# Optimization experiments

Hardware: AMD Instinct MI355X
Metric: run time of the kernel (lower is better)

The kernel has to match this reference:

```python
import jax, jax.numpy as jnp
from jax import lax
import numpy as np

DN = ('NCHW', 'OIHW', 'NCHW')

def conv(x, w, b, stride, pad):
    y = lax.conv_general_dilated(x, w, (stride, stride), [(pad, pad), (pad, pad)], dimension_numbers=DN)
    return y + b[None, :, None, None]

def conv_t(x, w, b):
    # torch ConvTranspose2d(k=4, s=2, p=1); w is torch layout [Cin, Cout, 4, 4]
    wf = jnp.flip(w, (2, 3)).transpose(1, 0, 2, 3)  # -> OIHW
    y = lax.conv_general_dilated(x, wf, (1, 1), [(2, 2), (2, 2)], lhs_dilation=(2, 2), dimension_numbers=DN)
    return y + b[None, :, None, None]

def setup_inputs() -> dict:
    key = jax.random.key(0)
    ks = jax.random.split(key, 20)
    B, C_in, H, W = 8, 1, 512, 512
    hid, zc, K = 64, 64, 512
    s = 0.05
    inp = {
        'x': jax.random.uniform(ks[0], (B, C_in, H, W), jnp.float32),
        # encoder: three 4x4 s2 convs + one 3x3 s1 conv
        'enc_w1': jax.random.normal(ks[1], (hid, C_in, 4, 4), jnp.float32) * s,
        'enc_b1': jnp.zeros((hid,), jnp.float32),
        'enc_w2': jax.random.normal(ks[2], (hid, hid, 4, 4), jnp.float32) * s,
        'enc_b2': jnp.zeros((hid,), jnp.float32),
        'enc_w3': jax.random.normal(ks[3], (hid, hid, 4, 4), jnp.float32) * s,
        'enc_b3': jnp.zeros((hid,), jnp.float32),
        'enc_w4': jax.random.normal(ks[4], (zc, hid, 3, 3), jnp.float32) * s,
        'enc_b4': jnp.zeros((zc,), jnp.float32),
        # codebook, uniform(-1/K, 1/K) as in torch init
        'codebook': jax.random.uniform(ks[5], (K, zc), jnp.float32, -1.0 / K, 1.0 / K),
        # decoder: 3x3 s1 conv + three 4x4 s2 conv-transposes (torch [Cin,Cout,kH,kW] layout)
        'dec_w1': jax.random.normal(ks[6], (hid, zc, 3, 3), jnp.float32) * s,
        'dec_b1': jnp.zeros((hid,), jnp.float32),
        'dec_tw1': jax.random.normal(ks[7], (hid, hid, 4, 4), jnp.float32) * s,
        'dec_tb1': jnp.zeros((hid,), jnp.float32),
        'dec_tw2': jax.random.normal(ks[8], (hid, hid, 4, 4), jnp.float32) * s,
        'dec_tb2': jnp.zeros((hid,), jnp.float32),
        'dec_tw3': jax.random.normal(ks[9], (hid, C_in, 4, 4), jnp.float32) * s,
        'dec_tb3': jnp.zeros((C_in,), jnp.float32),
    }
    return inp

def _forward(x, enc_w1, enc_b1, enc_w2, enc_b2, enc_w3, enc_b3, enc_w4, enc_b4,
             codebook, dec_w1, dec_b1, dec_tw1, dec_tb1, dec_tw2, dec_tb2, dec_tw3, dec_tb3):
    # ---- encoder ----
    h = jax.nn.relu(conv(x, enc_w1, enc_b1, 2, 1))
    h = jax.nn.relu(conv(h, enc_w2, enc_b2, 2, 1))
    h = jax.nn.relu(conv(h, enc_w3, enc_b3, 2, 1))
    z = conv(h, enc_w4, enc_b4, 1, 1)  # [B, zc, H/8, W/8]
    # ---- vector quantizer ----
    B, C, Hh, Ww = z.shape
    z_flat = z.transpose(0, 2, 3, 1).reshape(-1, C)  # [N, C]
    dist = (jnp.sum(z_flat ** 2, axis=1, keepdims=True)
            + jnp.sum(codebook ** 2, axis=1)
            - 2.0 * z_flat @ codebook.T)  # [N, K]
    idx = jnp.argmin(dist, axis=1)
    z_q = codebook[idx].reshape(B, Hh, Ww, C).transpose(0, 3, 1, 2)
    sg = lax.stop_gradient
    vq_loss = jnp.mean((sg(z_q) - z) ** 2) + 0.25 * jnp.mean((z_q - sg(z)) ** 2)
    z_q = z + sg(z_q - z)  # straight-through
    # ---- decoder ----
    d = jax.nn.relu(conv(z_q, dec_w1, dec_b1, 1, 1))
    d = jax.nn.relu(conv_t(d, dec_tw1, dec_tb1))
    d = jax.nn.relu(conv_t(d, dec_tw2, dec_tb2))
    x_hat = jax.nn.sigmoid(conv_t(d, dec_tw3, dec_tb3))
    return x_hat, vq_loss

def reference(x, enc_w1, enc_b1, enc_w2, enc_b2, enc_w3, enc_b3, enc_w4, enc_b4,
              codebook, dec_w1, dec_b1, dec_tw1, dec_tb1, dec_tw2, dec_tb2, dec_tw3, dec_tb3):
    return _forward(x, enc_w1, enc_b1, enc_w2, enc_b2, enc_w3, enc_b3, enc_w4, enc_b4,
                    codebook, dec_w1, dec_b1, dec_tw1, dec_tb1, dec_tw2, dec_tb2, dec_tw3, dec_tb3)
```

## Files before the change

kernel.cpp:

```cpp
#include <hip/hip_runtime.h>
#include <math.h>


typedef __bf16 bf16x8_t __attribute__((ext_vector_type(8)));
typedef _Float16 f16x8_t __attribute__((ext_vector_type(8)));
typedef float f32x4_t __attribute__((ext_vector_type(4)));
typedef _Float16 h2_t __attribute__((ext_vector_type(2)));

union FragU { uint4 u; bf16x8_t b; };
union Frag16 { uint4 u; f16x8_t h; };

__device__ inline f32x4_t mfma16(bf16x8_t a, bf16x8_t b, f32x4_t c) {
    return __builtin_amdgcn_mfma_f32_16x16x32_bf16(a, b, c, 0, 0, 0);
}
__device__ inline f32x4_t mfma16h(f16x8_t a, f16x8_t b, f32x4_t c) {
    return __builtin_amdgcn_mfma_f32_16x16x32_f16(a, b, c, 0, 0, 0);
}

__device__ inline void gl_lds16(const void* g, void* l) {
    __builtin_amdgcn_global_load_lds((const __attribute__((address_space(1))) void*)g,
                                     (__attribute__((address_space(3))) void*)l, 16, 0, 0);
}

__device__ inline unsigned bf16rne(float f) {
    unsigned u = __float_as_uint(f);
    u += 0x7FFFu + ((u >> 16) & 1u);
    return u >> 16;
}
__device__ inline unsigned pack2(float lo, float hi) {
    return bf16rne(lo) | (bf16rne(hi) << 16);
}
__device__ inline unsigned pack2h(float lo, float hi) {
    union { h2_t h; unsigned u; } r;
    r.h[0] = (_Float16)lo; r.h[1] = (_Float16)hi;
    return r.u;
}
__device__ inline unsigned short f16bits(float v) {
    union { _Float16 h; unsigned short s; } x; x.h = (_Float16)v; return x.s;
}
__device__ inline float f16lo(unsigned u) {
    union { unsigned u; h2_t h; } x; x.u = u; return (float)x.h[0];
}
__device__ inline float f16hi(unsigned u) {
    union { unsigned u; h2_t h; } x; x.u = u; return (float)x.h[1];
}
__device__ inline float bl(unsigned u) { return __uint_as_float(u << 16); }
__device__ inline float bh(unsigned u) { return __uint_as_float(u & 0xffff0000u); }

#if defined(__has_builtin)
#if __has_builtin(__builtin_amdgcn_fdot2)
#define HAS_FDOT2 1
#endif
#endif

__device__ inline float dot2h(unsigned x, unsigned w, float a) {
#ifdef HAS_FDOT2
    union { unsigned u; h2_t h; } ax, bw;
    ax.u = x; bw.u = w;
    return __builtin_amdgcn_fdot2(ax.h, bw.h, a, false);
#else
    union { unsigned u; _Float16 h[2]; } ax, bw;
    ax.u = x; bw.u = w;
    a = fmaf((float)ax.h[0], (float)bw.h[0], a);
    return fmaf((float)ax.h[1], (float)bw.h[1], a);
#endif
}
__device__ inline float dot8(uint4 x, uint4 w, float a) {
    a = dot2h(x.x, w.x, a); a = dot2h(x.y, w.y, a);
    a = dot2h(x.z, w.z, a); a = dot2h(x.w, w.w, a);
    return a;
}

template<int NR, int KW_, int SW, int CIC, int SPT, int NT, int OUTM>
__global__ __launch_bounds__(256) void conv_mfma(
    const unsigned short* __restrict__ in, const unsigned short* __restrict__ wp,
    const float* __restrict__ bias, void* __restrict__ outp,
    int Hp, int Wp, int PS, int nchunks, int Cout, int ncog,
    int Hpo, int Wpo, int relu)
{
    constexpr int W_ST = SW * (SPT - 1) + KW_;
    constexpr int SLOTS_PP = CIC / 8;
    constexpr int ROW_SLOTS = W_ST * SLOTS_PP;
    constexpr int SEGS = (ROW_SLOTS + 63) / 64;
    constexpr int KT = NR * KW_;
    constexpr int CSTEPS = CIC / 32;
    __shared__ __align__(16) unsigned short sh[NR * W_ST * CIC];

    int t = threadIdx.x, lane = t & 63, wv = t >> 6;
    int bx = blockIdx.x;
    int owt = bx;
    int ohg = blockIdx.y;
    int bz = blockIdx.z; int nb = bz / ncog; int cog = bz % ncog;
    int ow0 = owt * SPT;
    int row0 = SW * ohg;
    int col0 = SW * ow0;
    int coh = wv & 1;
    int sph = wv >> 1;
    int m = lane & 15, g = lane >> 4;

    f32x4_t acc[2][NT];
#pragma unroll
    for (int a = 0; a < 2; ++a)
#pragma unroll
        for (int u2 = 0; u2 < NT; ++u2) acc[a][u2] = (f32x4_t){0.f, 0.f, 0.f, 0.f};

    for (int ch = 0; ch < nchunks; ++ch) {
        if (ch) __syncthreads();
        for (int u_ = wv; u_ < NR * SEGS; u_ += 4) {
            int r = u_ / SEGS, seg = u_ - r * SEGS;
            int slot = seg * 64 + lane;
            int p = slot / SLOTS_PP;
            int uu = slot & (SLOTS_PP - 1);
            if (p < W_ST) {
                int su = (uu - (p & 7)) & (SLOTS_PP - 1);
                const unsigned short* gsrc = in +
                    (((size_t)nb * Hp + (row0 + r)) * Wp + (col0 + p)) * PS + ch * CIC + su * 8;
                unsigned short* ldst = sh + ((size_t)(r * ROW_SLOTS + seg * 64 + lane)) * 8;
                gl_lds16(gsrc, ldst);
            }
        }
        __syncthreads();
        int sbase = ch * (KT * CSTEPS);
#pragma unroll
        for (int tap = 0; tap < KT; ++tap) {
            const int r_l = tap / KW_, kwp = tap % KW_;
#pragma unroll
            for (int cs = 0; cs < CSTEPS; ++cs) {
                int s = sbase + tap * CSTEPS + cs;
                const uint4* wr = (const uint4*)wp + (size_t)(s * 4 + g) * Cout + cog * 64 + coh * 32 + m;
                FragU a0, a1;
                a0.u = wr[0];
                a1.u = wr[16];
#pragma unroll
                for (int u2 = 0; u2 < NT; ++u2) {
                    int sp_l = sph * (SPT / 2) + u2 * 16 + m;
                    int p = SW * sp_l + kwp;
                    int off = (cs * 32 + g * 8 + ((p & 7) << 3)) & (CIC - 1);
                    FragU bb;
                    bb.u = *(const uint4*)(sh + (size_t)(r_l * W_ST + p) * CIC + off);
                    acc[0][u2] = mfma16(a0.b, bb.b, acc[0][u2]);
                    acc[1][u2] = mfma16(a1.b, bb.b, acc[1][u2]);
                }
            }
        }
    }
#pragma unroll
    for (int a = 0; a < 2; ++a) {
        int co = cog * 64 + coh * 32 + a * 16 + g * 4;
        float4 bv = *(const float4*)(bias + co);
#pragma unroll
        for (int u2 = 0; u2 < NT; ++u2) {
            int ow = ow0 + sph * (SPT / 2) + u2 * 16 + m;
            float v0 = acc[a][u2][0] + bv.x;
            float v1 = acc[a][u2][1] + bv.y;
            float v2 = acc[a][u2][2] + bv.z;
            float v3 = acc[a][u2][3] + bv.w;
            if (relu) {
                v0 = fmaxf(v0, 0.f); v1 = fmaxf(v1, 0.f);
                v2 = fmaxf(v2, 0.f); v3 = fmaxf(v3, 0.f);
            }
            unsigned short* ob = (unsigned short*)outp;
            uint2 st;
            if constexpr (OUTM == 3) st = (uint2){pack2h(v0, v1), pack2h(v2, v3)};
            else                     st = (uint2){pack2(v0, v1), pack2(v2, v3)};
            *(uint2*)(ob + (((size_t)nb * Hpo + ohg + 1) * Wpo + (ow + 1)) * 64
                      + (coh * 32 + a * 16 + g * 4)) = st;
        }
    }
}

__global__ __launch_bounds__(256) void k_enc2w(
    const unsigned short* __restrict__ in, const unsigned short* __restrict__ wp,
    const float* __restrict__ bias, unsigned short* __restrict__ out)
{
    __shared__ __align__(16) unsigned short sh[16512];
    int t = threadIdx.x, lane = t & 63, wv = t >> 6;
    int m = lane & 15, g = lane >> 4;
    int ohg = blockIdx.x, n = blockIdx.y;

    f32x4_t acc[4][2];
#pragma unroll
    for (int a = 0; a < 4; ++a)
#pragma unroll
        for (int u2 = 0; u2 < 2; ++u2) acc[a][u2] = (f32x4_t){0.f, 0.f, 0.f, 0.f};

    const uint4* wp4 = (const uint4*)wp;
#pragma unroll
    for (int kh = 0; kh < 4; ++kh) {
        if (kh) __syncthreads();
        const unsigned short* rowp = in + ((size_t)(n * 258 + 2 * ohg + kh) * 258) * 64;
        for (int q = t; q < 2064; q += 256) {
            int p = q >> 3, uu = q & 7;
            int su = (uu - ((p >> 1) & 7)) & 7;
            gl_lds16(rowp + (size_t)p * 64 + su * 8, sh + (size_t)q * 8);
        }
        __syncthreads();
#pragma unroll
        for (int kwp = 0; kwp < 4; ++kwp) {
#pragma unroll
            for (int cs = 0; cs < 2; ++cs) {
                int s = (kh * 4 + kwp) * 2 + cs;
                const uint4* wr = wp4 + (size_t)(s * 4 + g) * 64 + m;
                FragU A[4];
#pragma unroll
                for (int a = 0; a < 4; ++a) A[a].u = wr[a * 16];
#pragma unroll
                for (int u2 = 0; u2 < 2; ++u2) {
                    int sp_l = wv * 32 + u2 * 16 + m;
                    int p = 2 * sp_l + kwp;
                    int rot = (sp_l + (kwp >> 1)) & 7;
                    int off = (cs * 32 + g * 8 + rot * 8) & 63;
                    FragU B;
                    B.u = *(const uint4*)(sh + (size_t)p * 64 + off);
#pragma unroll
                    for (int a = 0; a < 4; ++a)
                        acc[a][u2] = mfma16(A[a].b, B.b, acc[a][u2]);
                }
            }
        }
    }
#pragma unroll
    for (int a = 0; a < 4; ++a) {
        float4 bv = *(const float4*)(bias + a * 16 + g * 4);
#pragma unroll
        for (int u2 = 0; u2 < 2; ++u2) {
            int ow = wv * 32 + u2 * 16 + m;
            float v0 = fmaxf(acc[a][u2][0] + bv.x, 0.f);
            float v1 = fmaxf(acc[a][u2][1] + bv.y, 0.f);
            float v2 = fmaxf(acc[a][u2][2] + bv.z, 0.f);
            float v3 = fmaxf(acc[a][u2][3] + bv.w, 0.f);
            uint2 st = {pack2(v0, v1), pack2(v2, v3)};
            *(uint2*)(out + ((size_t)(n * 130 + ohg + 1) * 130 + ow + 1) * 64
                      + a * 16 + g * 4) = st;
        }
    }
}

template<int OUTM>
__global__ __launch_bounds__(256) void k_convtf(
    const unsigned short* __restrict__ in, const unsigned short* __restrict__ wp,
    const float* __restrict__ bias, unsigned short* __restrict__ out,
    int Hpi, int Wpi, int Hpo, int Wpo)
{
    __shared__ __align__(16) unsigned short sh[12672];
    int t = threadIdx.x, lane = t & 63, wv = t >> 6;
    int m = lane & 15, g = lane >> 4;
    int ph = wv >> 1, pw = wv & 1;
    int owt = blockIdx.x, ohg = blockIdx.y, n = blockIdx.z;
    int col0 = owt * 64;

    const unsigned short* an = in + ((size_t)(n * Hpi + ohg) * Wpi + col0) * 64;
    for (int q = t; q < 1584; q += 256) {
        int r = q / 528, rest = q - r * 528;
        int p = rest >> 3, uu = rest & 7;
        int su = (uu - (p & 7)) & 7;
        gl_lds16(an + ((size_t)r * Wpi + p) * 64 + su * 8, sh + (size_t)q * 8);
    }
    f32x4_t acc[4][4];
#pragma unroll
    for (int a = 0; a < 4; ++a)
#pragma unroll
        for (int u2 = 0; u2 < 4; ++u2) acc[a][u2] = (f32x4_t){0.f, 0.f, 0.f, 0.f};
    __syncthreads();

    const uint4* ws4 = (const uint4*)(wp + (size_t)(ph * 2 + pw) * 16384);
#pragma unroll
    for (int jh = 0; jh < 2; ++jh) {
#pragma unroll
        for (int jw = 0; jw < 2; ++jw) {
#pragma unroll
            for (int cs = 0; cs < 2; ++cs) {
                int s = (jh * 2 + jw) * 2 + cs;
                const uint4* wr = ws4 + (size_t)(s * 4 + g) * 64 + m;
                FragU A[4];
#pragma unroll
                for (int a = 0; a < 4; ++a) A[a].u = wr[a * 16];
                int r_l = ph + jh;
#pragma unroll
                for (int u2 = 0; u2 < 4; ++u2) {
                    int p = u2 * 16 + m + pw + jw;
                    int off = (cs * 32 + g * 8 + ((p & 7) << 3)) & 63;
                    FragU B;
                    B.u = *(const uint4*)(sh + (size_t)(r_l * 528 + p * 8) * 8 + off);
#pragma unroll
                    for (int a = 0; a < 4; ++a)
                        acc[a][u2] = mfma16(A[a].b, B.b, acc[a][u2]);
                }
            }
        }
    }
    int oho = 2 * ohg + ph;
#pragma unroll
    for (int a = 0; a < 4; ++a) {
        float4 bv = *(const float4*)(bias + a * 16 + g * 4);
#pragma unroll
        for (int u2 = 0; u2 < 4; ++u2) {
            int owo = 2 * (col0 + u2 * 16 + m) + pw;
            float v0 = fmaxf(acc[a][u2][0] + bv.x, 0.f);
            float v1 = fmaxf(acc[a][u2][1] + bv.y, 0.f);
            float v2 = fmaxf(acc[a][u2][2] + bv.z, 0.f);
            float v3 = fmaxf(acc[a][u2][3] + bv.w, 0.f);
            uint2 st;
            if constexpr (OUTM == 3) st = (uint2){pack2h(v0, v1), pack2h(v2, v3)};
            else                     st = (uint2){pack2(v0, v1), pack2(v2, v3)};
            *(uint2*)(out + ((size_t)(n * Hpo + oho + 1) * Wpo + owo + 1) * 64
                      + a * 16 + g * 4) = st;
        }
    }
}

__global__ __launch_bounds__(256) void k_enc4(
    const unsigned short* __restrict__ a3, const unsigned short* __restrict__ wp,
    const float* __restrict__ bias, unsigned short* __restrict__ zH,
    unsigned short* __restrict__ zL)
{
    __shared__ __align__(16) unsigned short sh[16896];
    int t = threadIdx.x, lane = t & 63, wv = t >> 6;
    int wc = wv & 1, wr = wv >> 1;
    int m = lane & 15, g = lane >> 4;
    int L = blockIdx.x;
    int xcd = L & 7, j = L >> 3;
    int cog = j & 3;
    int rt = (j >> 2) + xcd * 32;
    int row0 = rt * 128;
    int n = row0 >> 12;
    int oh0 = (row0 & 4095) >> 6;

    const unsigned short* an = a3 + ((size_t)(n * 66 + oh0) * 66) * 64;
    for (int seg = wv; seg < 33; seg += 4) {
        int slot = seg * 64 + lane;
        if (slot < 2112) {
            int r = slot / 528, rest = slot - r * 528;
            int p = rest >> 3, uu = rest & 7;
            int su = (uu - p) & 7;
            gl_lds16(an + ((size_t)(r * 66 + p)) * 64 + su * 8, sh + (size_t)slot * 8);
        }
    }
    f32x4_t acc[4][4];
#pragma unroll
    for (int a = 0; a < 4; ++a)
#pragma unroll
        for (int b = 0; b < 4; ++b) acc[a][b] = (f32x4_t){0.f, 0.f, 0.f, 0.f};
    __syncthreads();

#pragma unroll
    for (int tap = 0; tap < 9; ++tap) {
        const int kh = tap / 3, kwp = tap % 3;
#pragma unroll
        for (int cs = 0; cs < 2; ++cs) {
            int s = tap * 2 + cs;
            const uint4* wr4 = (const uint4*)wp + (size_t)(s * 4 + g) * 512 + cog * 128 + wc * 64 + m;
            FragU A[4];
#pragma unroll
            for (int ci = 0; ci < 4; ++ci) A[ci].u = wr4[ci * 16];
#pragma unroll
            for (int si = 0; si < 4; ++si) {
                int sp_l = wr * 64 + si * 16 + m;
                int r_l = (sp_l >> 6) + kh;
                int px = (sp_l & 63) + kwp;
                int off = (cs * 4 + g + px) & 7;
                FragU B;
                B.u = *(const uint4*)(sh + ((size_t)(r_l * 528 + px * 8 + off)) * 8);
#pragma unroll
                for (int ci = 0; ci < 4; ++ci)
                    acc[ci][si] = mfma16(A[ci].b, B.b, acc[ci][si]);
            }
        }
    }
    float4 bv[4];
#pragma unroll
    for (int ci = 0; ci < 4; ++ci)
        bv[ci] = *(const float4*)(bias + cog * 128 + wc * 64 + ci * 16 + g * 4);

    __syncthreads();
#pragma unroll
    for (int ci = 0; ci < 4; ++ci) {
#pragma unroll
        for (int si = 0; si < 4; ++si) {
            float v0 = acc[ci][si][0] + bv[ci].x;
            float v1 = acc[ci][si][1] + bv[ci].y;
            float v2 = acc[ci][si][2] + bv[ci].z;
            float v3 = acc[ci][si][3] + bv[ci].w;
            unsigned h0 = pack2h(v0, v1);
            unsigned h1 = pack2h(v2, v3);
            int row = wr * 64 + si * 16 + m;
            int col = wc * 64 + ci * 16 + g * 4;
            *(uint2*)(sh + (size_t)row * 132 + col) = (uint2){h0, h1};
        }
    }
    __syncthreads();
#pragma unroll
    for (int i = 0; i < 8; ++i) {
        int idx = i * 256 + t;
        int row = idx >> 4, c16 = idx & 15;
        uint4 v = *(const uint4*)(sh + (size_t)row * 132 + c16 * 8);
        int col = cog * 128 + c16 * 8;
        int sblk = col >> 5, off = col & 31;
        *(uint4*)(zH + ((size_t)sblk * 32768 + row0 + row) * 32 + off) = v;
    }
    __syncthreads();
#pragma unroll
    for (int ci = 0; ci < 4; ++ci) {
#pragma unroll
        for (int si = 0; si < 4; ++si) {
            float v0 = acc[ci][si][0] + bv[ci].x;
            float v1 = acc[ci][si][1] + bv[ci].y;
            float v2 = acc[ci][si][2] + bv[ci].z;
            float v3 = acc[ci][si][3] + bv[ci].w;
            unsigned h0 = pack2h(v0, v1);
            unsigned h1 = pack2h(v2, v3);
            unsigned l0 = pack2h(v0 - f16lo(h0), v1 - f16hi(h0));
            unsigned l1 = pack2h(v2 - f16lo(h1), v3 - f16hi(h1));
            int row = wr * 64 + si * 16 + m;
            int col = wc * 64 + ci * 16 + g * 4;
            *(uint2*)(sh + (size_t)row * 132 + col) = (uint2){l0, l1};
        }
    }
    __syncthreads();
#pragma unroll
    for (int i = 0; i < 8; ++i) {
        int idx = i * 256 + t;
        int row = idx >> 4, c16 = idx & 15;
        uint4 v = *(const uint4*)(sh + (size_t)row * 132 + c16 * 8);
        int col = cog * 128 + c16 * 8;
        int sblk = col >> 5, off = col & 31;
        *(uint4*)(zL + ((size_t)sblk * 32768 + row0 + row) * 32 + off) = v;
    }
}

__global__ __launch_bounds__(256) void k_halo_all(
    unsigned short* a1, unsigned short* a2, unsigned short* a3,
    unsigned short* zq, unsigned short* d1)
{
    unsigned short* buf; int Hp, Wp, PS;
    switch (blockIdx.z) {
        case 0: buf = a1; Hp = 258; Wp = 258; PS = 64; break;
        case 1: buf = a2; Hp = 130; Wp = 130; PS = 64; break;
        case 2: buf = a3; Hp = 66; Wp = 66; PS = 64; break;
        case 3: buf = zq; Hp = 66; Wp = 66; PS = 512; break;
        default: buf = d1; Hp = 66; Wp = 66; PS = 64; break;
    }
    int per = 2 * Wp + 2 * (Hp - 2);
    int chunks = PS >> 3;
    int total = per * chunks;
    int n = blockIdx.y;
    for (int i = blockIdx.x * 256 + threadIdx.x; i < total; i += gridDim.x * 256) {
        int pix = i / chunks, c = i - pix * chunks;
        int h, w;
        if (pix < Wp) { h = 0; w = pix; }
        else if (pix < 2 * Wp) { h = Hp - 1; w = pix - Wp; }
        else { int q = pix - 2 * Wp; h = 1 + (q >> 1); w = (q & 1) ? (Wp - 1) : 0; }
        uint4 zz = {0, 0, 0, 0};
        *(uint4*)(buf + (((size_t)n * Hp + h) * Wp + w) * PS + c * 8) = zz;
    }
}

__device__ inline void prep_conv_dev(const float* __restrict__ w,
    unsigned short* __restrict__ o, int Cout, int Cin, int T, int CIC, int idx)
{
    if (idx >= Cout * Cin * T) return;
    int tap = idx % T; int r = idx / T; int ci = r % Cin; int co = r / Cin;
    int chunk = ci / CIC, cil = ci % CIC;
    int k = chunk * (T * CIC) + tap * CIC + cil;
    int s = k >> 5, g = (k >> 3) & 3, j = k & 7;
    o[((size_t)(s * 4 + g) * Cout + co) * 8 + j] = (unsigned short)bf16rne(w[idx]);
}

__device__ inline void prep_wT_dev(const float* __restrict__ w,
    unsigned short* __restrict__ o, int idx)
{
    if (idx >= 65536) return;
    int ci = idx & 63; int r = idx >> 6;
    int jw = r & 1; r >>= 1;
    int jh = r & 1; r >>= 1;
    int co = r & 63; r >>= 6;
    int pw = r & 1; int ph = (r >> 1) & 1;
    int kh = (1 - ph) + 2 * (1 - jh);
    int kw = (1 - pw) + 2 * (1 - jw);
    int k = (jh * 2 + jw) * 64 + ci;
    int s = k >> 5, g = (k >> 3) & 3, j = k & 7;
    o[(size_t)(ph * 2 + pw) * 16384 + ((size_t)(s * 4 + g) * 64 + co) * 8 + j] =
        (unsigned short)bf16rne(w[((ci * 64 + co) * 4 + kh) * 4 + kw]);
}

__global__ __launch_bounds__(256) void k_prep_all(
    const float* __restrict__ enc_w2, const float* __restrict__ enc_w3,
    const float* __restrict__ enc_w4, const float* __restrict__ dec_w1,
    const float* __restrict__ tw1, const float* __restrict__ tw2,
    const float* __restrict__ cb,
    unsigned short* __restrict__ wA2, unsigned short* __restrict__ wA3,
    unsigned short* __restrict__ wB1, unsigned short* __restrict__ wB2,
    unsigned short* __restrict__ wC1, unsigned short* __restrict__ wC2,
    unsigned short* __restrict__ cbF,
    float* __restrict__ cn2)
{
    int idx = blockIdx.x * 256 + threadIdx.x;
    switch (blockIdx.y) {
    case 0: prep_conv_dev(enc_w2, wA2, 64, 64, 16, 64, idx); break;
    case 1: prep_conv_dev(enc_w3, wA3, 64, 64, 16, 64, idx); break;
    case 2: prep_conv_dev(enc_w4, wB1, 512, 64, 9, 64, idx); break;
    case 3: prep_conv_dev(dec_w1, wB2, 64, 512, 9, 128, idx); break;
    case 4: prep_wT_dev(tw1, wC1, idx); break;
    case 5: prep_wT_dev(tw2, wC2, idx); break;
    case 6: {
        if (idx < 262144) {
            int c = idx & 511, k = idx >> 9;
            int cblk = k >> 7, kl = k & 127, s = c >> 5, g = (c >> 3) & 3, j = c & 7;
            size_t off = ((((size_t)cblk * 16 + s) * 4 + g) * 128 + kl) * 8 + j;
            cbF[off] = f16bits(cb[idx]);
        }
    } break;
    default: {
        int code = blockIdx.x * 4 + (threadIdx.x >> 6);
        if (code < 512) {
            int l = threadIdx.x & 63;
            float s = 0.f;
#pragma unroll
            for (int i = 0; i < 8; ++i) {
                float v = cb[code * 512 + l + i * 64];
                s = fmaf(v, v, s);
            }
#pragma unroll
            for (int off = 32; off > 0; off >>= 1) s += __shfl_xor(s, off);
            if (l == 0) cn2[code] = 0.5f * s;
        }
    } break;
    }
}

__global__ __launch_bounds__(256) void k_conv1(const float* __restrict__ x,
    const float* __restrict__ w, const float* __restrict__ b, unsigned short* __restrict__ out)
{
    __shared__ float ws[1024];
    __shared__ float bs[64];
    int t = threadIdx.x;
#pragma unroll
    for (int i = 0; i < 4; ++i) ws[t + 256 * i] = w[t + 256 * i];
    if (t < 64) bs[t] = b[t];
    __syncthreads();
    int oh = blockIdx.x;
    int n = blockIdx.y;
    int ow = t;
    const float* xn = x + (size_t)n * 262144;
    float xv[16];
#pragma unroll
    for (int kh = 0; kh < 4; ++kh) {
        int ih = 2 * oh - 1 + kh;
        bool rok = (unsigned)ih < 512u;
        int ihc = min(max(ih, 0), 511);
#pragma unroll
        for (int kw = 0; kw < 4; ++kw) {
            int iw = 2 * ow - 1 + kw;
            bool ok = rok && ((unsigned)iw < 512u);
            int iwc = min(max(iw, 0), 511);
            float v = xn[ihc * 512 + iwc];
            xv[kh * 4 + kw] = ok ? v : 0.f;
        }
    }
    unsigned short* on = out + (((size_t)n * 258 + oh + 1) * 258 + (ow + 1)) * 64;
    unsigned uo[32];
#pragma unroll
    for (int co2 = 0; co2 < 32; ++co2) {
        float a0 = bs[2 * co2], a1 = bs[2 * co2 + 1];
#pragma unroll
        for (int q = 0; q < 16; ++q) {
            a0 = fmaf(xv[q], ws[(2 * co2) * 16 + q], a0);
            a1 = fmaf(xv[q], ws[(2 * co2 + 1) * 16 + q], a1);
        }
        uo[co2] = pack2(fmaxf(a0, 0.f), fmaxf(a1, 0.f));
    }
#pragma unroll
    for (int i = 0; i < 8; ++i) {
        uint4 st = {uo[4 * i], uo[4 * i + 1], uo[4 * i + 2], uo[4 * i + 3]};
        *(uint4*)(on + i * 8) = st;
    }
}

__device__ inline bool better_sc(float av, int ai, float bv, int bi) {
    return av > bv || (av == bv && ai < bi);
}

__global__ __launch_bounds__(256) void k_vqgemm(
    const unsigned short* __restrict__ zH, const unsigned short* __restrict__ cbF,
    const float* __restrict__ cn2, int* __restrict__ candI)
{
    __shared__ __align__(16) unsigned short shA[20480];
    int t = threadIdx.x, lane = t & 63, wv = t >> 6;
    int wc = wv & 1, wr = wv >> 1;
    int m = lane & 15, g = lane >> 4;
    int L = blockIdx.x;
    int xcd = L & 7, kk = L >> 3;
    int cblk = kk & 3;
    int row0 = ((kk >> 2) + xcd * 32) * 128;

    f32x4_t acc[4][4];
#pragma unroll
    for (int a = 0; a < 4; ++a)
#pragma unroll
        for (int b = 0; b < 4; ++b) acc[a][b] = (f32x4_t){0.f, 0.f, 0.f, 0.f};

    const uint4* bF = (const uint4*)cbF + (size_t)cblk * 8192;

    for (int c = 0; c < 4; ++c) {
        __syncthreads();
        for (int q = t; q < 2560; q += 256) {
            int ss = q / 640, rest = q - ss * 640;
            int r = rest / 5, seg = rest - r * 5;
            int s = c * 4 + ss;
            gl_lds16(zH + ((size_t)s * 32768 + row0 + r) * 32 + (seg & 3) * 8,
                     shA + (size_t)q * 8);
        }
        __syncthreads();
#pragma unroll
        for (int ss = 0; ss < 4; ++ss) {
            int s = c * 4 + ss;
            Frag16 B[4];
#pragma unroll
            for (int ni = 0; ni < 4; ++ni)
                B[ni].u = bF[(s * 4 + g) * 128 + wc * 64 + ni * 16 + m];
#pragma unroll
            for (int mi = 0; mi < 4; ++mi) {
                Frag16 A;
                A.u = *(const uint4*)(shA + (size_t)(ss * 5120 + (wr * 64 + mi * 16 + m) * 40 + g * 8));
#pragma unroll
                for (int ni = 0; ni < 4; ++ni)
                    acc[mi][ni] = mfma16h(A.h, B[ni].h, acc[mi][ni]);
            }
        }
    }
    __syncthreads();
    float* tV = (float*)shA;
    int*   tI = (int*)(shA + 2048);
    float c2[4];
#pragma unroll
    for (int ni = 0; ni < 4; ++ni) c2[ni] = cn2[cblk * 128 + wc * 64 + ni * 16 + m];
#pragma unroll
    for (int mi = 0; mi < 4; ++mi) {
#pragma unroll
        for (int r = 0; r < 4; ++r) {
            float v1 = -3e38f, v2 = -3e38f; int i1 = 0, i2 = 0;
#pragma unroll
            for (int ni = 0; ni < 4; ++ni) {
                float v = acc[mi][ni][r] - c2[ni];
                int ix = cblk * 128 + wc * 64 + ni * 16 + m;
                if (better_sc(v, ix, v1, i1)) { v2 = v1; i2 = i1; v1 = v; i1 = ix; }
                else if (better_sc(v, ix, v2, i2)) { v2 = v; i2 = ix; }
            }
#pragma unroll
            for (int off = 1; off < 16; off <<= 1) {
                float o1 = __shfl_xor(v1, off); int oi1 = __shfl_xor(i1, off);
                float o2 = __shfl_xor(v2, off); int oi2 = __shfl_xor(i2, off);
                if (better_sc(o1, oi1, v1, i1)) {
                    float nv2; int ni2;
                    if (better_sc(v1, i1, o2, oi2)) { nv2 = v1; ni2 = i1; }
                    else { nv2 = o2; ni2 = oi2; }
                    v1 = o1; i1 = oi1; v2 = nv2; i2 = ni2;
                } else if (better_sc(o1, oi1, v2, i2)) { v2 = o1; i2 = oi1; }
            }
            if (m == 0) {
                int row = wr * 64 + mi * 16 + g * 4 + r;
                tV[(wc * 128 + row) * 2 + 0] = v1; tI[(wc * 128 + row) * 2 + 0] = i1;
                tV[(wc * 128 + row) * 2 + 1] = v2; tI[(wc * 128 + row) * 2 + 1] = i2;
            }
        }
    }
    __syncthreads();
    if (t < 128) {
        float v1 = tV[t * 2], v2 = tV[t * 2 + 1];
        int i1 = tI[t * 2], i2 = tI[t * 2 + 1];
        float o1 = tV[(128 + t) * 2], o2 = tV[(128 + t) * 2 + 1];
        int oi1 = tI[(128 + t) * 2], oi2 = tI[(128 + t) * 2 + 1];
        if (better_sc(o1, oi1, v1, i1)) {
            float nv2; int ni2;
            if (better_sc(v1, i1, o2, oi2)) { nv2 = v1; ni2 = i1; }
            else { nv2 = o2; ni2 = oi2; }
            v1 = o1; i1 = oi1; v2 = nv2; i2 = ni2;
        } else if (better_sc(o1, oi1, v2, i2)) { v2 = o1; i2 = oi1; }
        candI[((size_t)cblk * 2 + 0) * 32768 + row0 + t] = i1;
        candI[((size_t)cblk * 2 + 1) * 32768 + row0 + t] = i2;
    }
}

__global__ __launch_bounds__(256) void k_vqfinal(
    const unsigned short* __restrict__ zH, const unsigned short* __restrict__ zL,
    const float* __restrict__ cb, const int* __restrict__ candI,
    unsigned short* __restrict__ zq, float* __restrict__ mind)
{
    int t = threadIdx.x, lane = t & 63, wv = t >> 6;
    int row = blockIdx.x * 4 + wv;
    size_t zoff = ((size_t)(lane >> 2) * 32768 + row) * 32 + (lane & 3) * 8;
    uint4 hu = *(const uint4*)(zH + zoff);
    uint4 lu = *(const uint4*)(zL + zoff);
    float z0 = f16lo(hu.x) + f16lo(lu.x);
    float z1 = f16hi(hu.x) + f16hi(lu.x);
    float z2 = f16lo(hu.y) + f16lo(lu.y);
    float z3 = f16hi(hu.y) + f16hi(lu.y);
    float z4 = f16lo(hu.z) + f16lo(lu.z);
    float z5 = f16hi(hu.z) + f16hi(lu.z);
    float z6 = f16lo(hu.w) + f16lo(lu.w);
    float z7 = f16hi(hu.w) + f16hi(lu.w);
    int mycand = (lane < 8) ? candI[(size_t)lane * 32768 + row] : 0;
    int cands[8];
    float d[8];
#pragma unroll
    for (int s = 0; s < 8; ++s) cands[s] = __shfl(mycand, s);
#pragma unroll
    for (int s = 0; s < 8; ++s) {
        const float* cr = cb + (size_t)cands[s] * 512 + lane * 8;
        float4 c0 = *(const float4*)cr;
        float4 c1 = *(const float4*)(cr + 4);
        float e, dd = 0.f;
        e = z0 - c0.x; dd = fmaf(e, e, dd);
        e = z1 - c0.y; dd = fmaf(e, e, dd);
        e = z2 - c0.z; dd = fmaf(e, e, dd);
        e = z3 - c0.w; dd = fmaf(e, e, dd);
        e = z4 - c1.x; dd = fmaf(e, e, dd);
        e = z5 - c1.y; dd = fmaf(e, e, dd);
        e = z6 - c1.z; dd = fmaf(e, e, dd);
        e = z7 - c1.w; dd = fmaf(e, e, dd);
        d[s] = dd;
    }
#pragma unroll
    for (int off = 1; off < 64; off <<= 1) {
#pragma unroll
        for (int s = 0; s < 8; ++s) d[s] += __shfl_xor(d[s], off);
    }
    float bd = d[0]; int bi_ = cands[0];
#pragma unroll
    for (int s = 1; s < 8; ++s) {
        if (d[s] < bd || (d[s] == bd && cands[s] < bi_)) { bd = d[s]; bi_ = cands[s]; }
    }
    {
        int n = row >> 12, hw = row & 4095, h = hw >> 6, w = hw & 63;
        const float* src = cb + (size_t)bi_ * 512 + lane * 8;
        float4 v0 = *(const float4*)src, v1 = *(const float4*)(src + 4);
        uint4 st = {pack2(v0.x, v0.y), pack2(v0.z, v0.w),
                    pack2(v1.x, v1.y), pack2(v1.z, v1.w)};
        *(uint4*)(zq + (((size_t)n * 66 + h + 1) * 66 + (w + 1)) * 512 + lane * 8) = st;
    }
    if (lane == 0) mind[row] = bd;
}

__global__ __launch_bounds__(256) void k_convt_final2(const unsigned short* __restrict__ xp,
    const float* __restrict__ w, const float* __restrict__ b, float* __restrict__ out)
{
    __shared__ __align__(16) unsigned short shx[3 * 1040 * 8];
    __shared__ __align__(16) unsigned wp[16][32];
    int t = threadIdx.x, lane = t & 63, wv = t >> 6;
    int bx = blockIdx.x, q = blockIdx.y, n = blockIdx.z;
    int colbase = bx * 128;
#pragma unroll
    for (int i = 0; i < 2; ++i) {
        int qq = t + i * 256;
        int tap = qq >> 5, c2 = qq & 31;
        wp[tap][c2] = pack2h(w[(2 * c2) * 16 + tap], w[(2 * c2 + 1) * 16 + tap]);
    }
    const unsigned short* an = xp + (size_t)n * 258 * 258 * 64;
    for (int u_ = wv; u_ < 51; u_ += 4) {
        int r = u_ / 17, seg = u_ % 17;
        int slot = seg * 64 + lane;
        if (slot < 1040) {
            int p = slot >> 3, uu = slot & 7;
            int su = (uu - p) & 7;
            int row = min(2 * q + r, 257);
            const unsigned short* gsrc = an + ((size_t)row * 258 + colbase + p) * 64 + su * 8;
            gl_lds16(gsrc, shx + ((size_t)(r * 1040 + slot)) * 8);
        }
    }
    __syncthreads();
    int ow = bx * 256 + t;
    int kwA = (ow + 1) & 1;
    int cA = ((ow + 1) >> 1) + 1 - colbase;
    int cB = cA - 1;
    float b0 = b[0];
    float acc0 = b0, acc1 = b0, acc2 = b0, acc3 = b0;
#pragma unroll
    for (int c8 = 0; c8 < 8; ++c8) {
        uint4 xr[3][2];
#pragma unroll
        for (int r = 0; r < 3; ++r) {
            xr[r][0] = *(const uint4*)(shx + (size_t)(r * 1040 + cB * 8 + ((c8 + cB) & 7)) * 8);
            xr[r][1] = *(const uint4*)(shx + (size_t)(r * 1040 + cA * 8 + ((c8 + cA) & 7)) * 8);
        }
        uint4 wA[4], wB[4];
#pragma unroll
        for (int kh = 0; kh < 4; ++kh) {
            wA[kh] = *(const uint4*)&wp[kh * 4 + kwA][c8 * 4];
            wB[kh] = *(const uint4*)&wp[kh * 4 + kwA + 2][c8 * 4];
        }
        acc0 = dot8(xr[1][1], wA[0], acc0); acc0 = dot8(xr[1][0], wB[0], acc0);
        acc0 = dot8(xr[0][1], wA[2], acc0); acc0 = dot8(xr[0][0], wB[2], acc0);
        acc1 = dot8(xr[1][1], wA[1], acc1); acc1 = dot8(xr[1][0], wB[1], acc1);
        acc1 = dot8(xr[0][1], wA[3], acc1); acc1 = dot8(xr[0][0], wB[3], acc1);
        acc2 = dot8(xr[2][1], wA[0], acc2); acc2 = dot8(xr[2][0], wB[0], acc2);
        acc2 = dot8(xr[1][1], wA[2], acc2); acc2 = dot8(xr[1][0], wB[2], acc2);
        acc3 = dot8(xr[2][1], wA[1], acc3); acc3 = dot8(xr[2][0], wB[1], acc3);
        acc3 = dot8(xr[1][1], wA[3], acc3); acc3 = dot8(xr[1][0], wB[3], acc3);
    }
    float accs[4] = {acc0, acc1, acc2, acc3};
    float* on = out + (size_t)n * 262144;
#pragma unroll
    for (int ro = 0; ro < 4; ++ro) {
        int oh = 4 * q - 1 + ro;
        if ((unsigned)oh < 512u)
            on[(size_t)oh * 512 + ow] = 1.0f / (1.0f + __expf(-accs[ro]));
    }
}

__global__ __launch_bounds__(256) void k_loss_final(const float* __restrict__ mind,
    float* __restrict__ out)
{
    __shared__ float redd[4];
    int t = threadIdx.x;
    float s = 0.f;
#pragma unroll 4
    for (int i = 0; i < 32; ++i) {
        float4 v = *(const float4*)(mind + i * 1024 + t * 4);
        s += v.x + v.y + v.z + v.w;
    }
#pragma unroll
    for (int off = 1; off < 64; off <<= 1) s += __shfl_xor(s, off);
    if ((t & 63) == 0) redd[t >> 6] = s;
    __syncthreads();
    if (t == 0)
        out[0] = 1.25f * (redd[0] + redd[1] + redd[2] + redd[3]) * (1.0f / 16777216.0f);
}

extern "C" void kernel_launch(void* const* d_in, const int* in_sizes, int n_in,
                              void* d_out, int out_size, void* d_ws, size_t ws_size,
                              hipStream_t stream)
{
    const float* x      = (const float*)d_in[0];
    const float* enc_w1 = (const float*)d_in[1];
    const float* enc_b1 = (const float*)d_in[2];
    const float* enc_w2 = (const float*)d_in[3];
    const float* enc_b2 = (const float*)d_in[4];
    const float* enc_w3 = (const float*)d_in[5];
    const float* enc_b3 = (const float*)d_in[6];
    const float* enc_w4 = (const float*)d_in[7];
    const float* enc_b4 = (const float*)d_in[8];
    const float* cb     = (const float*)d_in[9];
    const float* dec_w1 = (const float*)d_in[10];
    const float* dec_b1 = (const float*)d_in[11];
    const float* tw1    = (const float*)d_in[12];
    const float* tb1    = (const float*)d_in[13];
    const float* tw2    = (const float*)d_in[14];
    const float* tb2    = (const float*)d_in[15];
    const float* tw3    = (const float*)d_in[16];
    const float* tb3    = (const float*)d_in[17];
    float* out = (float*)d_out;

    unsigned short* a1 = (unsigned short*)d_ws;
    unsigned short* a2 = a1 + 34076672;
    unsigned short* a3 = a2 + 8652800;
    unsigned short* zH = a3 + 2230272;
    unsigned short* zL = zH + 16777216;
    unsigned short* zq = zL + 16777216;
    unsigned short* d1 = zq + 17842176;
    unsigned short* wA2 = d1 + 2230272;
    unsigned short* wA3 = wA2 + 65536;
    unsigned short* wB1 = wA3 + 65536;
    unsigned short* wB2 = wB1 + 294912;
    unsigned short* wC1 = wB2 + 294912;
    unsigned short* wC2 = wC1 + 65536;
    unsigned short* cbF = wC2 + 65536;
    float* cn2 = (float*)(cbF + 262144);
    int*   candI = (int*)(cn2 + 512);
    float* mind = (float*)(candI + 262144);

    k_halo_all<<<dim3(65, 8, 5), 256, 0, stream>>>(a1, a2, a3, zq, d1);
    k_prep_all<<<dim3(1152, 8), 256, 0, stream>>>(
        enc_w2, enc_w3, enc_w4, dec_w1, tw1, tw2, cb,
        wA2, wA3, wB1, wB2, wC1, wC2, cbF, cn2);

    k_conv1<<<dim3(256, 8), 256, 0, stream>>>(x, enc_w1, enc_b1, a1);
    k_enc2w<<<dim3(128, 8), 256, 0, stream>>>(a1, wA2, enc_b2, a2);
    conv_mfma<4, 4, 2, 64, 32, 1, 0><<<dim3(2, 64, 8), 256, 0, stream>>>(
        a2, wA3, enc_b3, a3, 130, 130, 64, 1, 64, 1, 66, 66, 1);
    k_enc4<<<1024, 256, 0, stream>>>(a3, wB1, enc_b4, zH, zL);
    k_vqgemm<<<1024, 256, 0, stream>>>(zH, cbF, cn2, candI);
    k_vqfinal<<<8192, 256, 0, stream>>>(zH, zL, cb, candI, zq, mind);
    conv_mfma<3, 3, 1, 128, 64, 2, 0><<<dim3(1, 64, 8), 256, 0, stream>>>(
        zq, wB2, dec_b1, d1, 66, 66, 512, 4, 64, 1, 66, 66, 1);
    k_convtf<0><<<dim3(1, 64, 8), 256, 0, stream>>>(d1, wC1, tb1, a2, 66, 66, 130, 130);
    k_convtf<3><<<dim3(2, 128, 8), 256, 0, stream>>>(a2, wC2, tb2, a1, 130, 130, 258, 258);
    k_convt_final2<<<dim3(2, 129, 8), 256, 0, stream>>>(a1, tw3, tb3, out);
    k_loss_final<<<1, 256, 0, stream>>>(mind, out + 2097152);
}
```

Baseline: 465.0 us.

## Double-buffer LDS staging in decoder conv and halve spatial tile

Adds an optional double-buffered LDS path to the MFMA conv kernel so the next channel chunk is loaded via global_load_lds while the current chunk is computed. The decoder 3x3 conv switches to this path and also halves the spatial tile per block (SPT 64->32, NT 2->1), doubling the grid to 1024 blocks. The aim is to hide load latency and raise occupancy. The cost is extra LDS per block, less weight-fragment reuse across spatial tiles, and more redundant halo loads.

```diff
diff --git a/kernel.cpp b/kernel.cpp
--- a/kernel.cpp
+++ b/kernel.cpp
@@ -71,7 +71,7 @@
     return a;
 }
 
-template<int NR, int KW_, int SW, int CIC, int SPT, int NT, int OUTM>
+template<int NR, int KW_, int SW, int CIC, int SPT, int NT, int OUTM, int DBUF>
 __global__ __launch_bounds__(256) void conv_mfma(
     const unsigned short* __restrict__ in, const unsigned short* __restrict__ wp,
     const float* __restrict__ bias, void* __restrict__ outp,
@@ -84,7 +84,8 @@
     constexpr int SEGS = (ROW_SLOTS + 63) / 64;
     constexpr int KT = NR * KW_;
     constexpr int CSTEPS = CIC / 32;
-    __shared__ __align__(16) unsigned short sh[NR * W_ST * CIC];
+    constexpr int BUFSZ = NR * W_ST * CIC;
+    __shared__ __align__(16) unsigned short sh[(DBUF ? 2 : 1) * BUFSZ];
 
     int t = threadIdx.x, lane = t & 63, wv = t >> 6;
     int bx = blockIdx.x;
@@ -104,8 +105,7 @@
 #pragma unroll
         for (int u2 = 0; u2 < NT; ++u2) acc[a][u2] = (f32x4_t){0.f, 0.f, 0.f, 0.f};
 
-    for (int ch = 0; ch < nchunks; ++ch) {
-        if (ch) __syncthreads();
+    auto stage = [&](int ch, unsigned short* buf) {
         for (int u_ = wv; u_ < NR * SEGS; u_ += 4) {
             int r = u_ / SEGS, seg = u_ - r * SEGS;
             int slot = seg * 64 + lane;
@@ -115,11 +115,13 @@
                 int su = (uu - (p & 7)) & (SLOTS_PP - 1);
                 const unsigned short* gsrc = in +
                     (((size_t)nb * Hp + (row0 + r)) * Wp + (col0 + p)) * PS + ch * CIC + su * 8;
-                unsigned short* ldst = sh + ((size_t)(r * ROW_SLOTS + seg * 64 + lane)) * 8;
+                unsigned short* ldst = buf + ((size_t)(r * ROW_SLOTS + seg * 64 + lane)) * 8;
                 gl_lds16(gsrc, ldst);
             }
         }
-        __syncthreads();
+    };
+
+    auto compute = [&](int ch, const unsigned short* buf) {
         int sbase = ch * (KT * CSTEPS);
 #pragma unroll
         for (int tap = 0; tap < KT; ++tap) {
@@ -137,11 +139,27 @@
                     int p = SW * sp_l + kwp;
                     int off = (cs * 32 + g * 8 + ((p & 7) << 3)) & (CIC - 1);
                     FragU bb;
-                    bb.u = *(const uint4*)(sh + (size_t)(r_l * W_ST + p) * CIC + off);
+                    bb.u = *(const uint4*)(buf + (size_t)(r_l * W_ST + p) * CIC + off);
                     acc[0][u2] = mfma16(a0.b, bb.b, acc[0][u2]);
                     acc[1][u2] = mfma16(a1.b, bb.b, acc[1][u2]);
                 }
             }
+        }
+    };
+
+    stage(0, sh);
+    __syncthreads();
+    for (int ch = 0; ch < nchunks; ++ch) {
+        if constexpr (DBUF != 0) {
+            if (ch + 1 < nchunks) stage(ch + 1, sh + (size_t)((ch + 1) & 1) * BUFSZ);
+        }
+        compute(ch, DBUF ? (sh + (size_t)(ch & 1) * BUFSZ) : sh);
+        if (ch + 1 < nchunks) {
+            if constexpr (DBUF == 0) {
+                __syncthreads();
+                stage(ch + 1, sh);
+            }
+            __syncthreads();
         }
     }
 #pragma unroll
@@ -875,12 +893,12 @@
 
     k_conv1<<<dim3(256, 8), 256, 0, stream>>>(x, enc_w1, enc_b1, a1);
     k_enc2w<<<dim3(128, 8), 256, 0, stream>>>(a1, wA2, enc_b2, a2);
-    conv_mfma<4, 4, 2, 64, 32, 1, 0><<<dim3(2, 64, 8), 256, 0, stream>>>(
+    conv_mfma<4, 4, 2, 64, 32, 1, 0, 0><<<dim3(2, 64, 8), 256, 0, stream>>>(
         a2, wA3, enc_b3, a3, 130, 130, 64, 1, 64, 1, 66, 66, 1);
     k_enc4<<<1024, 256, 0, stream>>>(a3, wB1, enc_b4, zH, zL);
     k_vqgemm<<<1024, 256, 0, stream>>>(zH, cbF, cn2, candI);
     k_vqfinal<<<8192, 256, 0, stream>>>(zH, zL, cb, candI, zq, mind);
-    conv_mfma<3, 3, 1, 128, 64, 2, 0><<<dim3(1, 64, 8), 256, 0, stream>>>(
+    conv_mfma<3, 3, 1, 128, 32, 1, 0, 1><<<dim3(2, 64, 8), 256, 0, stream>>>(
         zq, wB2, dec_b1, d1, 66, 66, 512, 4, 64, 1, 66, 66, 1);
     k_convtf<0><<<dim3(1, 64, 8), 256, 0, stream>>>(d1, wC1, tb1, a2, 66, 66, 130, 130);
     k_convtf<3><<<dim3(2, 128, 8), 256, 0, stream>>>(a2, wC2, tb2, a1, 130, 130, 258, 258);
```

Measured after the change: 481.2 us. 1.03x slower.
